# Kernel tuning notes

Hardware: AMD Instinct MI355X
Metric: run time of the kernel (lower is better)

Reference implementation:

```python
import jax, jax.numpy as jnp
import numpy as np

VOCAB = 5000
HIDDEN = 512
BATCH = 64
SEQ = 256


def setup_inputs() -> dict:
    key = jax.random.key(0)
    ks = jax.random.split(key, 8)
    s = 0.02
    return {
        "X": jax.random.randint(ks[0], (BATCH, SEQ), 0, VOCAB),
        "state": jnp.zeros((1, BATCH, HIDDEN), jnp.float32),
        # PyTorch GRU params: weight_ih (3H, V), weight_hh (3H, H), biases (3H,)
        "W_ih": jax.random.normal(ks[1], (3 * HIDDEN, VOCAB), jnp.float32) * s,
        "W_hh": jax.random.normal(ks[2], (3 * HIDDEN, HIDDEN), jnp.float32) * s,
        "b_ih": jax.random.normal(ks[3], (3 * HIDDEN,), jnp.float32) * s,
        "b_hh": jax.random.normal(ks[4], (3 * HIDDEN,), jnp.float32) * s,
        # dense: Linear(hidden, vocab)
        "W_out": jax.random.normal(ks[5], (VOCAB, HIDDEN), jnp.float32) * s,
        "b_out": jax.random.normal(ks[6], (VOCAB,), jnp.float32) * s,
    }


def reference(X, state, W_ih, W_hh, b_ih, b_hh, W_out, b_out):
    V = W_ih.shape[1]
    H = W_hh.shape[1]
    # d2l.to_onehot + torch.stack -> (seq, batch, vocab), seq-first for GRU
    onehot = jax.nn.one_hot(X.T, V, dtype=W_ih.dtype)  # (S, B, V)
    # input-side GEMM for all timesteps at once (cuDNN does the same batching)
    x_proj = jnp.einsum('sbv,gv->sbg', onehot, W_ih) + b_ih  # (S, B, 3H)

    h0 = state[0]  # (B, H)

    def step(h, xp):
        gi_r, gi_z, gi_n = jnp.split(xp, 3, axis=-1)
        gh = h @ W_hh.T + b_hh
        gh_r, gh_z, gh_n = jnp.split(gh, 3, axis=-1)
        r = jax.nn.sigmoid(gi_r + gh_r)
        z = jax.nn.sigmoid(gi_z + gh_z)
        n = jnp.tanh(gi_n + r * gh_n)
        h_new = (1.0 - z) * n + z * h
        return h_new, h_new

    hT, Y = jax.lax.scan(step, h0, x_proj)  # Y: (S, B, H)
    out = Y.reshape(-1, H) @ W_out.T + b_out  # (S*B, V)
    return out, hT[None]  # state shape (1, B, H)
```

## Files before the change

kernel.cpp:

```cpp
#include <hip/hip_runtime.h>

typedef __attribute__((ext_vector_type(8))) short bf16x8;
typedef __attribute__((ext_vector_type(4))) float f32x4;
typedef __attribute__((ext_vector_type(4))) int i32x4;
typedef __attribute__((ext_vector_type(2))) unsigned int u32x2;
typedef unsigned short ushort_t;
typedef unsigned int uint_t;

#define VOCAB 5000
#define HID   512
#define B_    64
#define SEQ_  256
#define H3    1536
#define NPAD  5120
#define NREC  32
#define NGEM  224
#define NTILE (SEQ_ * 40)

__device__ __forceinline__ ushort_t f2bf(float f){
  uint_t u = __float_as_uint(f);
  u = u + 0x7fffu + ((u >> 16) & 1u);
  return (ushort_t)(u >> 16);
}
__device__ __forceinline__ float bf2f(ushort_t s){
  return __uint_as_float(((uint_t)s) << 16);
}

__device__ __forceinline__ uint_t agent_load_u32(const uint_t* p){
  uint_t v;
  asm volatile("global_load_dword %0, %1, off sc1\n\t"
               "s_waitcnt vmcnt(0)" : "=v"(v) : "v"(p) : "memory");
  return v;
}
__device__ __forceinline__ void agent_store_u32(uint_t* p, uint_t v){
  asm volatile("global_store_dword %0, %1, off sc1" :: "v"(p), "v"(v) : "memory");
}
__device__ __forceinline__ void agent_store_u64(ushort_t* p, u32x2 v){
  asm volatile("global_store_dwordx2 %0, %1, off sc1" :: "v"(p), "v"(v) : "memory");
}

__global__ void k_transpose(const float* __restrict__ W, float* __restrict__ WT){
  __shared__ float tile[32][33];
  const int bv = blockIdx.x * 32;
  const int bg = blockIdx.y * 32;
  const int tx = threadIdx.x, ty = threadIdx.y;
  #pragma unroll
  for(int r = 0; r < 32; r += 8){
    int g = bg + ty + r, v = bv + tx;
    tile[ty + r][tx] = (v < VOCAB) ? W[(size_t)g * VOCAB + v] : 0.f;
  }
  __syncthreads();
  #pragma unroll
  for(int r = 0; r < 32; r += 8){
    int v = bv + ty + r, g = bg + tx;
    if(v < VOCAB) WT[(size_t)v * H3 + g] = tile[tx][ty + r];
  }
}

__global__ void k_cvt_wout(const float* __restrict__ W, ushort_t* __restrict__ WP){
  int idx = (blockIdx.x * 256 + threadIdx.x) * 4;
  if(idx >= NPAD * HID) return;
  float x0 = 0.f, x1 = 0.f, x2 = 0.f, x3 = 0.f;
  if(idx < VOCAB * HID){
    const float4 v = *(const float4*)(W + idx);
    x0 = v.x; x1 = v.y; x2 = v.z; x3 = v.w;
  }
  ushort4 o; o.x = f2bf(x0); o.y = f2bf(x1); o.z = f2bf(x2); o.w = f2bf(x3);
  *(ushort4*)(WP + idx) = o;
}

__global__ void k_gather(const int* __restrict__ X, const float* __restrict__ WT,
                         const float* __restrict__ bih, ushort_t* __restrict__ xp){
  const int sb = blockIdx.x;
  const int s = sb >> 6, b = sb & 63;
  const int x = X[b * SEQ_ + s];
  const float4* src = (const float4*)(WT + (size_t)x * H3);
  const float4* bi  = (const float4*)bih;
  for(int i = threadIdx.x; i < H3 / 4; i += 256){
    float4 v = src[i], c = bi[i];
    ushort4 o;
    o.x = f2bf(v.x + c.x); o.y = f2bf(v.y + c.y);
    o.z = f2bf(v.z + c.z); o.w = f2bf(v.w + c.w);
    ((ushort4*)(xp + (size_t)sb * H3))[i] = o;
  }
}

__global__ void __launch_bounds__(256, 1) k_mega(
    const float* __restrict__ Whh, const float* __restrict__ bhh,
    const float* __restrict__ state, const ushort_t* __restrict__ xp,
    const ushort_t* __restrict__ WP, const float* __restrict__ bout,
    ushort_t* __restrict__ hbuf, ushort_t* __restrict__ Y,
    float* __restrict__ out, float* __restrict__ hT, uint_t* flags)
{
  __shared__ __align__(16) char smem[102912];
  const int bid = blockIdx.x, tid = threadIdx.x;
  const int lane = tid & 63, wv = tid >> 6;
  const int l15 = lane & 15, lhi = lane >> 4;

  if(bid < NREC){
    ushort_t (*tsc)[16][20] = (ushort_t(*)[16][20])(smem + 100224);
    const int g = bid;
    const int dom = g >> 3, sub = g & 7;
    const int jbwg = sub * 64;
    const int jg = wv;
    const int jt0 = jbwg + jg * 16;
    const int j  = jt0 + l15;
    const int bband = dom * 16;

    const float cr = bhh[j], cz = bhh[HID + j], cn = bhh[2 * HID + j];

    bf16x8 wb[48];
    #pragma unroll
    for(int gate = 0; gate < 3; gate++){
      #pragma unroll
      for(int kk = 0; kk < 16; kk++){
        const float* wsrc = Whh + (size_t)(gate * HID + j) * HID + kk * 32 + 8 * lhi;
        float4 w0 = *(const float4*)(wsrc);
        float4 w1 = *(const float4*)(wsrc + 4);
        bf16x8 bf;
        bf[0] = (short)f2bf(w0.x); bf[1] = (short)f2bf(w0.y);
        bf[2] = (short)f2bf(w0.z); bf[3] = (short)f2bf(w0.w);
        bf[4] = (short)f2bf(w1.x); bf[5] = (short)f2bf(w1.y);
        bf[6] = (short)f2bf(w1.z); bf[7] = (short)f2bf(w1.w);
        wb[gate * 16 + kk] = bf;
      }
    }

    float hprev[4]; int brow[4];
    #pragma unroll
    for(int i = 0; i < 4; i++){
      brow[i] = bband + lhi * 4 + i;
      hprev[i] = state[brow[i] * HID + j];
    }

    #pragma unroll
    for(int i = 0; i < 4; i++) tsc[wv][lhi * 4 + i][l15] = f2bf(hprev[i]);
    asm volatile("s_waitcnt lgkmcnt(0)" ::: "memory");
    {
      u32x2 rv = *(const u32x2*)&tsc[wv][l15][lhi * 4];
      agent_store_u64(hbuf + (size_t)(bband + l15) * HID + jt0 + lhi * 4, rv);
    }
    asm volatile("s_waitcnt vmcnt(0)" ::: "memory");
    __syncthreads();
    if(tid == 0) agent_store_u32(flags + g * 32, 1u);

    const int fidx = dom * 8 + ((lane + sub) & 7);
    const size_t roff = (size_t)(bband + l15) * HID + jt0 + lhi * 4;

    for(int t = 0; t < SEQ_; ++t){
      const ushort_t* hin  = hbuf + (t & 1) * (B_ * HID);
      ushort_t*       hout = hbuf + ((t + 1) & 1) * (B_ * HID);

      float gir[4], giz[4], gin_[4];
      const ushort_t* xr = xp + (size_t)t * B_ * H3;
      #pragma unroll
      for(int i = 0; i < 4; i++){
        const ushort_t* p = xr + (size_t)brow[i] * H3 + j;
        gir[i] = bf2f(p[0]); giz[i] = bf2f(p[HID]); gin_[i] = bf2f(p[2 * HID]);
      }

      if(lane < 8){
        const uint_t need = (uint_t)(t + 1);
        int gd = 0;
        while(agent_load_u32(flags + fidx * 32) < need){
          __builtin_amdgcn_s_sleep(1);
          if(++gd > 200000) break;
        }
      }

      i32x4 tmp[16];
      const char* abase = (const char*)(hin + (size_t)(bband + l15) * HID + 8 * lhi);
      #define LDH(i, off) asm volatile("global_load_dwordx4 %0, %1, off offset:" #off " sc1" \
                                       : "=v"(tmp[i]) : "v"(abase) : "memory");
      LDH(0,0)   LDH(1,64)   LDH(2,128)  LDH(3,192)
      LDH(4,256) LDH(5,320)  LDH(6,384)  LDH(7,448)
      LDH(8,512) LDH(9,576)  LDH(10,640) LDH(11,704)
      LDH(12,768) LDH(13,832) LDH(14,896) LDH(15,960)
      #undef LDH
      asm volatile("s_waitcnt vmcnt(0)" ::: "memory");
      __builtin_amdgcn_sched_barrier(0);

      f32x4 acc0 = {0.f,0.f,0.f,0.f}, acc1 = {0.f,0.f,0.f,0.f}, acc2 = {0.f,0.f,0.f,0.f};
      #pragma unroll
      for(int kk = 0; kk < 16; kk++){
        bf16x8 a = __builtin_bit_cast(bf16x8, tmp[kk]);
        acc0 = __builtin_amdgcn_mfma_f32_16x16x32_bf16(a, wb[kk],      acc0, 0, 0, 0);
        acc1 = __builtin_amdgcn_mfma_f32_16x16x32_bf16(a, wb[16 + kk], acc1, 0, 0, 0);
        acc2 = __builtin_amdgcn_mfma_f32_16x16x32_bf16(a, wb[32 + kk], acc2, 0, 0, 0);
      }

      float hn4[4];
      #pragma unroll
      for(int i = 0; i < 4; i++){
        float r = 1.f / (1.f + expf(-(gir[i] + acc0[i] + cr)));
        float z = 1.f / (1.f + expf(-(giz[i] + acc1[i] + cz)));
        float n = tanhf(gin_[i] + r * (acc2[i] + cn));
        hn4[i] = (1.f - z) * n + z * hprev[i];
        hprev[i] = hn4[i];
      }

      #pragma unroll
      for(int i = 0; i < 4; i++) tsc[wv][lhi * 4 + i][l15] = f2bf(hn4[i]);
      asm volatile("s_waitcnt lgkmcnt(0)" ::: "memory");
      {
        u32x2 rv = *(const u32x2*)&tsc[wv][l15][lhi * 4];
        agent_store_u64(hout + roff, rv);
        agent_store_u64(Y + (size_t)t * B_ * HID + roff, rv);
      }
      asm volatile("s_waitcnt vmcnt(0)" ::: "memory");
      __syncthreads();
      if(tid == 0) agent_store_u32(flags + g * 32, (uint_t)(t + 2));

      if(t == SEQ_ - 1){
        #pragma unroll
        for(int i = 0; i < 4; i++) hT[brow[i] * HID + j] = hn4[i];
      }
    }
  } else {
    ushort_t (*At)[520] = (ushort_t(*)[520])smem;
    const int gb = bid - NREC;

    for(int tile = gb; tile < NTILE; tile += NGEM){
      const int t = tile / 40, n0 = (tile % 40) * 128;

      if(wv == 0){
        const uint_t need = (uint_t)(t + 2);
        int gd = 0;
        while(true){
          uint_t v = 0xffffffffu;
          if(lane < 32) v = agent_load_u32(flags + lane * 32);
          if(__all(v >= need)) break;
          __builtin_amdgcn_s_sleep(64);
          if(++gd > 2000000) break;
        }
      }
      __syncthreads();

      {
        const int row = tid >> 2, q = tid & 3;
        const char* src = (const char*)(Y + (size_t)t * B_ * HID) + row * 1024 + q * 256;
        i32x4 tv[16];
        #define LDA(i, off) asm volatile("global_load_dwordx4 %0, %1, off offset:" #off " sc1" \
                                         : "=v"(tv[i]) : "v"(src) : "memory");
        LDA(0,0)   LDA(1,16)  LDA(2,32)  LDA(3,48)
        LDA(4,64)  LDA(5,80)  LDA(6,96)  LDA(7,112)
        LDA(8,128) LDA(9,144) LDA(10,160) LDA(11,176)
        LDA(12,192) LDA(13,208) LDA(14,224) LDA(15,240)
        #undef LDA
        asm volatile("s_waitcnt vmcnt(0)" ::: "memory");
        __builtin_amdgcn_sched_barrier(0);
        #pragma unroll
        for(int i = 0; i < 16; i++) *(i32x4*)&At[row][q * 128 + i * 8] = tv[i];
      }
      __syncthreads();

      f32x4 acc[4][2];
      #pragma unroll
      for(int a = 0; a < 4; a++){ acc[a][0] = (f32x4){0,0,0,0}; acc[a][1] = (f32x4){0,0,0,0}; }

      const ushort_t* B0 = WP + (size_t)(n0 + wv * 32 + l15) * HID;
      const ushort_t* B1 = WP + (size_t)(n0 + wv * 32 + 16 + l15) * HID;
      #pragma unroll
      for(int kt = 0; kt < 16; kt++){
        const int kc = kt * 32 + 8 * lhi;
        bf16x8 b0 = *(const bf16x8*)(B0 + kc);
        bf16x8 b1 = *(const bf16x8*)(B1 + kc);
        bf16x8 a0 = *(const bf16x8*)&At[0 * 16 + l15][kc];
        bf16x8 a1 = *(const bf16x8*)&At[1 * 16 + l15][kc];
        bf16x8 a2 = *(const bf16x8*)&At[2 * 16 + l15][kc];
        bf16x8 a3 = *(const bf16x8*)&At[3 * 16 + l15][kc];
        acc[0][0] = __builtin_amdgcn_mfma_f32_16x16x32_bf16(a0, b0, acc[0][0], 0, 0, 0);
        acc[0][1] = __builtin_amdgcn_mfma_f32_16x16x32_bf16(a0, b1, acc[0][1], 0, 0, 0);
        acc[1][0] = __builtin_amdgcn_mfma_f32_16x16x32_bf16(a1, b0, acc[1][0], 0, 0, 0);
        acc[1][1] = __builtin_amdgcn_mfma_f32_16x16x32_bf16(a1, b1, acc[1][1], 0, 0, 0);
        acc[2][0] = __builtin_amdgcn_mfma_f32_16x16x32_bf16(a2, b0, acc[2][0], 0, 0, 0);
        acc[2][1] = __builtin_amdgcn_mfma_f32_16x16x32_bf16(a2, b1, acc[2][1], 0, 0, 0);
        acc[3][0] = __builtin_amdgcn_mfma_f32_16x16x32_bf16(a3, b0, acc[3][0], 0, 0, 0);
        acc[3][1] = __builtin_amdgcn_mfma_f32_16x16x32_bf16(a3, b1, acc[3][1], 0, 0, 0);
      }

      #pragma unroll
      for(int mi = 0; mi < 4; mi++){
        #pragma unroll
        for(int ni = 0; ni < 2; ni++){
          const int v = n0 + wv * 32 + ni * 16 + l15;
          if(v < VOCAB){
            const float bb = bout[v];
            #pragma unroll
            for(int i = 0; i < 4; i++){
              const int sb = t * 64 + mi * 16 + lhi * 4 + i;
              out[(size_t)sb * VOCAB + v] = acc[mi][ni][i] + bb;
            }
          }
        }
      }
      __syncthreads();
    }
  }
}

extern "C" void kernel_launch(void* const* d_in, const int* in_sizes, int n_in,
                              void* d_out, int out_size, void* d_ws, size_t ws_size,
                              hipStream_t stream)
{
  const int*   X     = (const int*)  d_in[0];
  const float* state = (const float*)d_in[1];
  const float* Wih   = (const float*)d_in[2];
  const float* Whh   = (const float*)d_in[3];
  const float* bih   = (const float*)d_in[4];
  const float* bhh   = (const float*)d_in[5];
  const float* Wout  = (const float*)d_in[6];
  const float* bout  = (const float*)d_in[7];
  float* out = (float*)d_out;
  float* hT  = out + (size_t)SEQ_ * B_ * VOCAB;

  char* ws = (char*)d_ws;
  const size_t off_WihT  = 4096;
  const size_t off_WoutP = off_WihT  + (size_t)VOCAB * H3  * sizeof(float);
  const size_t off_Y     = off_WoutP + (size_t)NPAD  * HID * sizeof(ushort_t);
  const size_t off_h     = off_Y     + (size_t)SEQ_ * B_ * HID * sizeof(ushort_t);
  const size_t off_xp    = off_h     + (size_t)2 * B_ * HID * sizeof(ushort_t);

  uint_t*   flags = (uint_t*)  ws;
  float*    WihT  = (float*)   (ws + off_WihT);
  ushort_t* WoutP = (ushort_t*)(ws + off_WoutP);
  ushort_t* Ybuf  = (ushort_t*)(ws + off_Y);
  ushort_t* hbuf  = (ushort_t*)(ws + off_h);
  ushort_t* xp    = (ushort_t*)(ws + off_xp);

  (void)hipMemsetAsync(d_ws, 0, 4096, stream);
  hipLaunchKernelGGL(k_transpose, dim3(157, 48), dim3(32, 8), 0, stream, Wih, WihT);
  hipLaunchKernelGGL(k_cvt_wout, dim3((NPAD * HID / 4 + 255) / 256), dim3(256), 0, stream, Wout, WoutP);
  hipLaunchKernelGGL(k_gather, dim3(SEQ_ * B_), dim3(256), 0, stream, X, WihT, bih, xp);
  hipLaunchKernelGGL(k_mega, dim3(NREC + NGEM), dim3(256), 0, stream,
                     Whh, bhh, state, xp, WoutP, bout, hbuf, Ybuf, out, hT, flags);
}
```

Measured before the change: 1.211 ms.

## Use per-wave step flags, prefetch next-step gate inputs, use fast sigmoid/tanh

Each recurrent wave now publishes its own progress flag instead of waiting on a block-wide barrier, so a wave no longer stalls on its slowest sibling. Consumer waves poll all 32 per-wave flags of their batch domain, and the GEMM waves poll all 128. The input-projection values for step t+1 are loaded while step t's MFMAs run, taking those loads off the serial recurrence path. Sigmoid and tanh switch to __expf-based forms, which cuts latency at some cost in accuracy and adds more flag-polling traffic.

```diff
diff --git a/kernel.cpp b/kernel.cpp
--- a/kernel.cpp
+++ b/kernel.cpp
@@ -24,6 +24,13 @@
 }
 __device__ __forceinline__ float bf2f(ushort_t s){
   return __uint_as_float(((uint_t)s) << 16);
+}
+__device__ __forceinline__ float fast_sigmoid(float x){
+  return 1.f / (1.f + __expf(-x));
+}
+__device__ __forceinline__ float fast_tanh(float x){
+  float e = __expf(2.f * x);
+  return 1.f - 2.f / (e + 1.f);
 }
 
 __device__ __forceinline__ uint_t agent_load_u32(const uint_t* p){
@@ -106,6 +113,7 @@
     const int jt0 = jbwg + jg * 16;
     const int j  = jt0 + l15;
     const int bband = dom * 16;
+    uint_t* myflag = flags + (g * 4 + wv) * 32;
 
     const float cr = bhh[j], cz = bhh[HID + j], cn = bhh[2 * HID + j];
 
@@ -141,28 +149,26 @@
       agent_store_u64(hbuf + (size_t)(bband + l15) * HID + jt0 + lhi * 4, rv);
     }
     asm volatile("s_waitcnt vmcnt(0)" ::: "memory");
-    __syncthreads();
-    if(tid == 0) agent_store_u32(flags + g * 32, 1u);
-
-    const int fidx = dom * 8 + ((lane + sub) & 7);
+    if(lane == 0) agent_store_u32(myflag, 1u);
+
+    const int pfi = dom * 32 + ((lane + g) & 31);
     const size_t roff = (size_t)(bband + l15) * HID + jt0 + lhi * 4;
+
+    float gir[4], giz[4], gin_[4];
+    #pragma unroll
+    for(int i = 0; i < 4; i++){
+      const ushort_t* p = xp + (size_t)brow[i] * H3 + j;
+      gir[i] = bf2f(p[0]); giz[i] = bf2f(p[HID]); gin_[i] = bf2f(p[2 * HID]);
+    }
 
     for(int t = 0; t < SEQ_; ++t){
       const ushort_t* hin  = hbuf + (t & 1) * (B_ * HID);
       ushort_t*       hout = hbuf + ((t + 1) & 1) * (B_ * HID);
 
-      float gir[4], giz[4], gin_[4];
-      const ushort_t* xr = xp + (size_t)t * B_ * H3;
-      #pragma unroll
-      for(int i = 0; i < 4; i++){
-        const ushort_t* p = xr + (size_t)brow[i] * H3 + j;
-        gir[i] = bf2f(p[0]); giz[i] = bf2f(p[HID]); gin_[i] = bf2f(p[2 * HID]);
-      }
-
-      if(lane < 8){
+      if(lane < 32){
         const uint_t need = (uint_t)(t + 1);
         int gd = 0;
-        while(agent_load_u32(flags + fidx * 32) < need){
+        while(agent_load_u32(flags + pfi * 32) < need){
           __builtin_amdgcn_s_sleep(1);
           if(++gd > 200000) break;
         }
@@ -180,6 +186,16 @@
       asm volatile("s_waitcnt vmcnt(0)" ::: "memory");
       __builtin_amdgcn_sched_barrier(0);
 
+      float girn[4], gizn[4], ginn[4];
+      if(t + 1 < SEQ_){
+        const ushort_t* xrn = xp + (size_t)(t + 1) * B_ * H3;
+        #pragma unroll
+        for(int i = 0; i < 4; i++){
+          const ushort_t* p = xrn + (size_t)brow[i] * H3 + j;
+          girn[i] = bf2f(p[0]); gizn[i] = bf2f(p[HID]); ginn[i] = bf2f(p[2 * HID]);
+        }
+      }
+
       f32x4 acc0 = {0.f,0.f,0.f,0.f}, acc1 = {0.f,0.f,0.f,0.f}, acc2 = {0.f,0.f,0.f,0.f};
       #pragma unroll
       for(int kk = 0; kk < 16; kk++){
@@ -192,9 +208,9 @@
       float hn4[4];
       #pragma unroll
       for(int i = 0; i < 4; i++){
-        float r = 1.f / (1.f + expf(-(gir[i] + acc0[i] + cr)));
-        float z = 1.f / (1.f + expf(-(giz[i] + acc1[i] + cz)));
-        float n = tanhf(gin_[i] + r * (acc2[i] + cn));
+        float r = fast_sigmoid(gir[i] + acc0[i] + cr);
+        float z = fast_sigmoid(giz[i] + acc1[i] + cz);
+        float n = fast_tanh(gin_[i] + r * (acc2[i] + cn));
         hn4[i] = (1.f - z) * n + z * hprev[i];
         hprev[i] = hn4[i];
       }
@@ -208,8 +224,10 @@
         agent_store_u64(Y + (size_t)t * B_ * HID + roff, rv);
       }
       asm volatile("s_waitcnt vmcnt(0)" ::: "memory");
-      __syncthreads();
-      if(tid == 0) agent_store_u32(flags + g * 32, (uint_t)(t + 2));
+      if(lane == 0) agent_store_u32(myflag, (uint_t)(t + 2));
+
+      #pragma unroll
+      for(int i = 0; i < 4; i++){ gir[i] = girn[i]; giz[i] = gizn[i]; gin_[i] = ginn[i]; }
 
       if(t == SEQ_ - 1){
         #pragma unroll
@@ -227,9 +245,9 @@
         const uint_t need = (uint_t)(t + 2);
         int gd = 0;
         while(true){
-          uint_t v = 0xffffffffu;
-          if(lane < 32) v = agent_load_u32(flags + lane * 32);
-          if(__all(v >= need)) break;
+          uint_t v0 = agent_load_u32(flags + lane * 32);
+          uint_t v1 = agent_load_u32(flags + (lane + 64) * 32);
+          if(__all((v0 >= need) && (v1 >= need))) break;
           __builtin_amdgcn_s_sleep(64);
           if(++gd > 2000000) break;
         }
@@ -315,7 +333,7 @@
   float* hT  = out + (size_t)SEQ_ * B_ * VOCAB;
 
   char* ws = (char*)d_ws;
-  const size_t off_WihT  = 4096;
+  const size_t off_WihT  = 32768;
   const size_t off_WoutP = off_WihT  + (size_t)VOCAB * H3  * sizeof(float);
   const size_t off_Y     = off_WoutP + (size_t)NPAD  * HID * sizeof(ushort_t);
   const size_t off_h     = off_Y     + (size_t)SEQ_ * B_ * HID * sizeof(ushort_t);
@@ -328,7 +346,7 @@
   ushort_t* hbuf  = (ushort_t*)(ws + off_h);
   ushort_t* xp    = (ushort_t*)(ws + off_xp);
 
-  (void)hipMemsetAsync(d_ws, 0, 4096, stream);
+  (void)hipMemsetAsync(d_ws, 0, 32768, stream);
   hipLaunchKernelGGL(k_transpose, dim3(157, 48), dim3(32, 8), 0, stream, Wih, WihT);
   hipLaunchKernelGGL(k_cvt_wout, dim3((NPAD * HID / 4 + 255) / 256), dim3(256), 0, stream, Wout, WoutP);
   hipLaunchKernelGGL(k_gather, dim3(SEQ_ * B_), dim3(256), 0, stream, X, WihT, bih, xp);
```

Result: slower. 1.449 ms (+19.6%).
